# Optimization experiments

Hardware: AMD Instinct MI355X
Metric: run time of the kernel (lower is better)

## Reference

```python
import jax, jax.numpy as jnp
import numpy as np
import math

B, T, C = 2, 8192, 1024
H = 16
HD = C // H  # 64
WIN = 256    # local_window_size


def _rope_tables(T, hd):
    inv_freq = 1.0 / (10000.0 ** (np.arange(0, hd, 2, dtype=np.float32) / hd))
    t = np.arange(T, dtype=np.float32)
    freqs = np.outer(t, inv_freq)                      # [T, hd/2]
    emb = np.concatenate([freqs, freqs], axis=-1)      # [T, hd]
    return jnp.asarray(np.cos(emb))[None, None], jnp.asarray(np.sin(emb))[None, None]


def setup_inputs() -> dict:
    key = jax.random.key(0)
    ks = jax.random.split(key, 10)
    x = jax.random.normal(ks[0], (B, T, C), dtype=jnp.float32)
    # padding_mask: bool [B,T]; per the source, True positions end up masked out of attention
    padding_mask = jax.random.randint(ks[1], (B, T), 0, 2).astype(bool)
    cos, sin = _rope_tables(T, HD)                     # [1,1,T,HD]
    s = 1.0 / math.sqrt(C)
    Wq = jax.random.normal(ks[2], (C, C), dtype=jnp.float32) * s
    bq = jnp.zeros((C,), dtype=jnp.float32)
    Wk = jax.random.normal(ks[3], (C, C), dtype=jnp.float32) * s
    bk = jnp.zeros((C,), dtype=jnp.float32)
    Wv = jax.random.normal(ks[4], (C, C), dtype=jnp.float32) * s
    bv = jnp.zeros((C,), dtype=jnp.float32)
    Wo = jax.random.normal(ks[5], (C, C), dtype=jnp.float32) * s
    bo = jnp.zeros((C,), dtype=jnp.float32)
    return {"x": x, "padding_mask": padding_mask, "cos": cos, "sin": sin,
            "Wq": Wq, "bq": bq, "Wk": Wk, "bk": bk, "Wv": Wv, "bv": bv,
            "Wo": Wo, "bo": bo}


def _rotate_half(t):
    h = t.shape[-1] // 2
    return jnp.concatenate([-t[..., h:], t[..., :h]], axis=-1)


def reference(x, padding_mask, cos, sin, Wq, bq, Wk, bk, Wv, bv, Wo, bo):
    Bx, Tx, Cx = x.shape
    Wn = WIN
    pad_end = (Wn - Tx % Wn) % Wn            # static python int
    Tp = Tx + pad_end
    nW = Tp // Wn
    half = Wn // 2
    hd = cos.shape[-1]

    cos_t = jnp.broadcast_to(cos[0, 0][None], (Bx, Tx, hd))
    sin_t = jnp.broadcast_to(sin[0, 0][None], (Bx, Tx, hd))
    if pad_end > 0:
        x = jnp.pad(x, ((0, 0), (0, pad_end), (0, 0)))
        padding_mask = jnp.pad(padding_mask, ((0, 0), (0, pad_end)))
        cos_t = jnp.pad(cos_t, ((0, 0), (0, pad_end), (0, 0)))
        sin_t = jnp.pad(sin_t, ((0, 0), (0, pad_end), (0, 0)))

    # non-overlapping query windows: [B*nW, W, C]
    q_win = x.reshape(Bx * nW, Wn, Cx)
    cos_q = cos_t.reshape(Bx * nW, Wn, hd)[:, None]   # [Bw,1,W,hd]
    sin_q = sin_t.reshape(Bx * nW, Wn, hd)[:, None]

    # overlapping key/value windows of size 2W, stride W
    x_ctx = jnp.pad(x, ((0, 0), (half, half), (0, 0)))
    cos_ctx = jnp.pad(cos_t, ((0, 0), (half, half), (0, 0)))
    sin_ctx = jnp.pad(sin_t, ((0, 0), (half, half), (0, 0)))
    pk = jnp.pad(padding_mask, ((0, 0), (half, half)))  # pad value False
    idx = jnp.arange(nW)[:, None] * Wn + jnp.arange(2 * Wn)[None, :]  # [nW, 2W]
    k_win = x_ctx[:, idx].reshape(Bx * nW, 2 * Wn, Cx)
    cos_k = cos_ctx[:, idx].reshape(Bx * nW, 2 * Wn, hd)[:, None]
    sin_k = sin_ctx[:, idx].reshape(Bx * nW, 2 * Wn, hd)[:, None]
    pk = pk[:, idx].reshape(Bx * nW, 2 * Wn)

    # attn_mask: True = attend (SDPA bool-mask convention)
    attn_mask = ~pk
    all_attend = jnp.all(attn_mask, axis=-1)
    attn_mask = attn_mask.at[:, 0].set(jnp.where(all_attend, False, attn_mask[:, 0]))

    Bw = Bx * nW
    q = (q_win @ Wq.T + bq).reshape(Bw, Wn, H, HD).transpose(0, 2, 1, 3)        # [Bw,H,W,hd]
    k = (k_win @ Wk.T + bk).reshape(Bw, 2 * Wn, H, HD).transpose(0, 2, 1, 3)    # [Bw,H,2W,hd]
    v = (k_win @ Wv.T + bv).reshape(Bw, 2 * Wn, H, HD).transpose(0, 2, 1, 3)

    q = q * cos_q + _rotate_half(q) * sin_q
    k = k * cos_k + _rotate_half(k) * sin_k

    scale = 1.0 / math.sqrt(HD)
    scores = jnp.einsum('bhqd,bhkd->bhqk', q, k) * scale                        # [Bw,H,W,2W]
    scores = jnp.where(attn_mask[:, None, None, :], scores, jnp.finfo(scores.dtype).min)
    attn = jax.nn.softmax(scores, axis=-1)
    out = jnp.einsum('bhqk,bhkd->bhqd', attn, v)
    out = out.transpose(0, 2, 1, 3).reshape(Bw, Wn, Cx)
    out = out @ Wo.T + bo
    out = out.reshape(Bx, nW * Wn, Cx)[:, :Tx]
    return out
```

## Files before the change

### kernel.cpp

```cpp
#include <hip/hip_runtime.h>
#include <hip/hip_bf16.h>
#include <stdint.h>

#define T_SEQ 8192
#define B_SZ 2
#define CDIM 1024
#define NH 16
#define HDIM 64
#define NW 32

typedef unsigned short ushort_t;
typedef __attribute__((ext_vector_type(8))) short short8;
typedef __attribute__((ext_vector_type(8))) unsigned short us8;
typedef __attribute__((ext_vector_type(4))) unsigned short us4;
typedef __attribute__((ext_vector_type(4))) float f32x4;

__device__ __forceinline__ unsigned short f2bf(float f) {
  union { float f; unsigned int u; } c; c.f = f;
  return (unsigned short)((c.u + 0x7FFFu + ((c.u >> 16) & 1u)) >> 16);
}
__device__ __forceinline__ void gld16(void* lds, const void* g) {
  __builtin_amdgcn_global_load_lds(
      (const __attribute__((address_space(1))) void*)g,
      (__attribute__((address_space(3))) void*)lds, 16, 0, 0);
}

__global__ __launch_bounds__(256) void cvt_f32_bf16(const float* __restrict__ src,
                                                    ushort_t* __restrict__ dst, int n4)
{
  int i = blockIdx.x * 256 + threadIdx.x;
  if (i < n4) {
    float4 v = ((const float4*)src)[i];
    ushort4 o;
    o.x = f2bf(v.x); o.y = f2bf(v.y); o.z = f2bf(v.z); o.w = f2bf(v.w);
    ((ushort4*)dst)[i] = o;
  }
}

__global__ __launch_bounds__(256) void cvt_w4(const float* __restrict__ w0,
                                              const float* __restrict__ w1,
                                              const float* __restrict__ w2,
                                              const float* __restrict__ w3,
                                              ushort_t* __restrict__ dst)
{
  const float* srcs[4] = {w0, w1, w2, w3};
  const float* s = srcs[blockIdx.y];
  ushort_t* d = dst + (size_t)blockIdx.y * CDIM * CDIM;
  int i = blockIdx.x * 256 + threadIdx.x;
  float4 v = ((const float4*)s)[i];
  ushort4 o;
  o.x = f2bf(v.x); o.y = f2bf(v.y); o.z = f2bf(v.z); o.w = f2bf(v.w);
  ((ushort4*)d)[i] = o;
}

template <int EPI>
__global__ __launch_bounds__(256) void gemm_bt(const ushort_t* __restrict__ A,
                                               const ushort_t* __restrict__ W,
                                               const float* __restrict__ bias,
                                               void* __restrict__ OutP,
                                               const float* __restrict__ cosT,
                                               const float* __restrict__ sinT)
{
  __shared__ ushort_t As[128 * 32];
  __shared__ ushort_t Bs[128 * 32];
  const int t = threadIdx.x;
  const int lane = t & 63;
  const int wv = t >> 6;
  const int m0 = blockIdx.y * 128;
  const int n0 = blockIdx.x * 128;
  const int wm = (wv >> 1) * 64;
  const int wn = (wv & 1) * 64;

  f32x4 acc[4][4];
#pragma unroll
  for (int i = 0; i < 4; i++)
#pragma unroll
    for (int j = 0; j < 4; j++) acc[i][j] = (f32x4){0.f, 0.f, 0.f, 0.f};

  const int srow = t >> 2;
  const int scol = (t & 3) * 8;
  const ushort_t* Ag0 = A + (size_t)(m0 + srow) * CDIM + scol;
  const ushort_t* Ag1 = Ag0 + (size_t)64 * CDIM;
  const ushort_t* Wg0 = W + (size_t)(n0 + srow) * CDIM + scol;
  const ushort_t* Wg1 = Wg0 + (size_t)64 * CDIM;
  ushort_t* la0 = &As[srow * 32 + scol];
  ushort_t* la1 = &As[(srow + 64) * 32 + scol];
  ushort_t* lb0 = &Bs[srow * 32 + scol];
  ushort_t* lb1 = &Bs[(srow + 64) * 32 + scol];

  const int fr = lane & 15;
  const int kq = (lane >> 4) * 8;

  for (int kt = 0; kt < CDIM; kt += 32) {
    __syncthreads();
    gld16(la0, Ag0 + kt);
    gld16(la1, Ag1 + kt);
    gld16(lb0, Wg0 + kt);
    gld16(lb1, Wg1 + kt);
    __syncthreads();
    short8 a[4], b[4];
#pragma unroll
    for (int i = 0; i < 4; i++) a[i] = *(const short8*)&As[(wm + i * 16 + fr) * 32 + kq];
#pragma unroll
    for (int i = 0; i < 4; i++) b[i] = *(const short8*)&Bs[(wn + i * 16 + fr) * 32 + kq];
#pragma unroll
    for (int i = 0; i < 4; i++)
#pragma unroll
      for (int j = 0; j < 4; j++)
        acc[i][j] = __builtin_amdgcn_mfma_f32_16x16x32_bf16(a[i], b[j], acc[i][j], 0, 0, 0);
  }

  const int quad = lane >> 4;

  if constexpr (EPI == 1) {
    ushort_t* Out = (ushort_t*)OutP;
#pragma unroll
    for (int jp = 0; jp < 2; jp++) {
      int n_lo = n0 + wn + jp * 16 + fr;
      int n_hi = n_lo + 32;
      float bl = bias[n_lo], bh = bias[n_hi];
      int d = jp * 16 + fr;
#pragma unroll
      for (int i = 0; i < 4; i++) {
        int m = m0 + wm + i * 16 + quad * 4;
#pragma unroll
        for (int r = 0; r < 4; r++) {
          int tt = (m + r) & (T_SEQ - 1);
          float c = cosT[tt * HDIM + d];
          float sn = sinT[tt * HDIM + d];
          float lo = acc[i][jp][r] + bl;
          float hi = acc[i][jp + 2][r] + bh;
          Out[(size_t)(m + r) * CDIM + n_lo] = f2bf(lo * c - hi * sn);
          Out[(size_t)(m + r) * CDIM + n_hi] = f2bf(hi * c + lo * sn);
        }
      }
    }
  } else if constexpr (EPI == 2) {
    ushort_t* Out = (ushort_t*)OutP;
#pragma unroll
    for (int j = 0; j < 4; j++) {
      int n = n0 + wn + j * 16 + fr;
      float bvv = bias[n];
#pragma unroll
      for (int i = 0; i < 4; i++) {
        int m = m0 + wm + i * 16 + quad * 4;
        int bb = m >> 13;
        int tq = m & (T_SEQ - 1);
        us4 pk;
#pragma unroll
        for (int r = 0; r < 4; r++) pk[r] = f2bf(acc[i][j][r] + bvv);
        *(us4*)&Out[((size_t)bb * CDIM + n) * T_SEQ + tq] = pk;
      }
    }
  } else {
#pragma unroll
    for (int j = 0; j < 4; j++) {
      int n = n0 + wn + j * 16 + fr;
      float bvv = bias[n];
#pragma unroll
      for (int i = 0; i < 4; i++) {
        int m = m0 + wm + i * 16 + quad * 4;
#pragma unroll
        for (int r = 0; r < 4; r++) {
          if constexpr (EPI == 3)
            ((float*)OutP)[(size_t)(m + r) * CDIM + n] = acc[i][j][r] + bvv;
          else
            ((ushort_t*)OutP)[(size_t)(m + r) * CDIM + n] = f2bf(acc[i][j][r] + bvv);
        }
      }
    }
  }
}

__global__ __launch_bounds__(256) void attn_kernel(const ushort_t* __restrict__ Q,
                                                   const ushort_t* __restrict__ Kg,
                                                   const ushort_t* __restrict__ Vt,
                                                   const int* __restrict__ mask,
                                                   ushort_t* __restrict__ AO)
{
  __shared__ ushort_t Qs[128 * 72];
  __shared__ ushort_t Ks[64 * 72];
  __shared__ ushort_t Vts[64 * 72];
  __shared__ ushort_t Ps[4 * 16 * 72];
  __shared__ unsigned char att[512];

  const int t = threadIdx.x;
  const int lane = t & 63;
  const int wv = t >> 6;
  const int h = blockIdx.x;
  const int w = blockIdx.y >> 1;
  const int qh = blockIdx.y & 1;
  const int b = blockIdx.z;

  bool a0, a1;
  {
    int p0 = w * 256 + t - 128;
    a0 = (p0 < 0 || p0 >= T_SEQ) ? true : (mask[b * T_SEQ + p0] == 0);
    int p1 = p0 + 256;
    a1 = (p1 < 0 || p1 >= T_SEQ) ? true : (mask[b * T_SEQ + p1] == 0);
  }
  int all1 = __syncthreads_and((int)(a0 && a1));
  att[t] = a0 ? 1 : 0;
  att[t + 256] = a1 ? 1 : 0;
  if (all1 && t == 0) att[0] = 0;

  {
    int row = t >> 3;
    int c8 = (t & 7) * 8;
    size_t qbase = ((size_t)b * T_SEQ + w * 256 + qh * 128) * CDIM + h * HDIM + c8;
#pragma unroll
    for (int p = 0; p < 4; p++) {
      int r = p * 32 + row;
      *(us8*)&Qs[r * 72 + c8] = *(const us8*)&Q[qbase + (size_t)r * CDIM];
    }
  }

  const int fr = lane & 15;
  const int quad = lane >> 4;
  const int kq = quad * 8;
  const ushort_t* vt_base = Vt + ((size_t)b * CDIM + h * HDIM) * T_SEQ;

  float m_run[2][4], l_run[2][4];
  f32x4 o[2][4];
#pragma unroll
  for (int mt = 0; mt < 2; mt++)
#pragma unroll
    for (int r = 0; r < 4; r++) { m_run[mt][r] = -3.0e38f; l_run[mt][r] = 0.f; }
#pragma unroll
  for (int mt = 0; mt < 2; mt++)
#pragma unroll
    for (int nt = 0; nt < 4; nt++) o[mt][nt] = (f32x4){0.f, 0.f, 0.f, 0.f};

  for (int kc = 0; kc < 8; kc++) {
    __syncthreads();
    {
      int row = t >> 3;
      int c8 = (t & 7) * 8;
#pragma unroll
      for (int p = 0; p < 2; p++) {
        int jj = p * 32 + row;
        int pos = w * 256 + kc * 64 + jj - 128;
        us8 kval = (us8)(0);
        if (pos >= 0 && pos < T_SEQ)
          kval = *(const us8*)&Kg[((size_t)b * T_SEQ + pos) * CDIM + h * HDIM + c8];
        *(us8*)&Ks[jj * 72 + c8] = kval;
      }
    }
    {
      int dd = t >> 3;
      int kg = (t & 7) * 8;
      int pos0 = w * 256 + kc * 64 - 128 + kg;
      bool inr = (pos0 >= 0) && (pos0 < T_SEQ);
#pragma unroll
      for (int p = 0; p < 2; p++) {
        int d = p * 32 + dd;
        us8 vv = (us8)(0);
        if (inr) vv = *(const us8*)&vt_base[(size_t)d * T_SEQ + pos0];
        *(us8*)&Vts[d * 72 + kg] = vv;
      }
    }
    __syncthreads();

    short8 afr[2][2], bfr[4][2];
#pragma unroll
    for (int mt = 0; mt < 2; mt++)
#pragma unroll
      for (int ks = 0; ks < 2; ks++)
        afr[mt][ks] = *(const short8*)&Qs[(wv * 32 + mt * 16 + fr) * 72 + ks * 32 + kq];
#pragma unroll
    for (int nt = 0; nt < 4; nt++)
#pragma unroll
      for (int ks = 0; ks < 2; ks++)
        bfr[nt][ks] = *(const short8*)&Ks[(nt * 16 + fr) * 72 + ks * 32 + kq];

    f32x4 s[2][4];
#pragma unroll
    for (int mt = 0; mt < 2; mt++)
#pragma unroll
      for (int nt = 0; nt < 4; nt++) {
        f32x4 a = (f32x4){0.f, 0.f, 0.f, 0.f};
        a = __builtin_amdgcn_mfma_f32_16x16x32_bf16(afr[mt][0], bfr[nt][0], a, 0, 0, 0);
        a = __builtin_amdgcn_mfma_f32_16x16x32_bf16(afr[mt][1], bfr[nt][1], a, 0, 0, 0);
        s[mt][nt] = a;
      }

    bool at[4];
#pragma unroll
    for (int nt = 0; nt < 4; nt++) at[nt] = att[kc * 64 + nt * 16 + fr] != 0;
#pragma unroll
    for (int mt = 0; mt < 2; mt++)
#pragma unroll
      for (int nt = 0; nt < 4; nt++)
#pragma unroll
        for (int r = 0; r < 4; r++)
          s[mt][nt][r] = at[nt] ? s[mt][nt][r] * 0.125f : -3.0e38f;

#pragma unroll
    for (int mt = 0; mt < 2; mt++) {
#pragma unroll
      for (int r = 0; r < 4; r++) {
        float mm = fmaxf(fmaxf(s[mt][0][r], s[mt][1][r]), fmaxf(s[mt][2][r], s[mt][3][r]));
        for (int off = 1; off < 16; off <<= 1) mm = fmaxf(mm, __shfl_xor(mm, off, 64));
        float mnew = fmaxf(m_run[mt][r], mm);
        float alpha = __expf(m_run[mt][r] - mnew);
        float rs = 0.f;
#pragma unroll
        for (int nt = 0; nt < 4; nt++) {
          float p = __expf(s[mt][nt][r] - mnew);
          s[mt][nt][r] = p;
          rs += p;
        }
        for (int off = 1; off < 16; off <<= 1) rs += __shfl_xor(rs, off, 64);
        l_run[mt][r] = l_run[mt][r] * alpha + rs;
        m_run[mt][r] = mnew;
#pragma unroll
        for (int nt = 0; nt < 4; nt++) o[mt][nt][r] *= alpha;
      }
    }

    short8 vf[4][2];
#pragma unroll
    for (int nt = 0; nt < 4; nt++)
#pragma unroll
      for (int ks = 0; ks < 2; ks++)
        vf[nt][ks] = *(const short8*)&Vts[(nt * 16 + fr) * 72 + ks * 32 + kq];

    ushort_t* pw = &Ps[wv * 16 * 72];
    const int rot_r = 8 * (fr >> 2);
#pragma unroll
    for (int mt = 0; mt < 2; mt++) {
#pragma unroll
      for (int nt = 0; nt < 4; nt++) {
#pragma unroll
        for (int r = 0; r < 4; r++) {
          int cs = ((nt * 16 + fr) + 8 * quad) & 63;
          pw[(quad * 4 + r) * 72 + cs] = f2bf(s[mt][nt][r]);
        }
      }
      short8 pf[2];
#pragma unroll
      for (int ks = 0; ks < 2; ks++)
        pf[ks] = *(const short8*)&pw[fr * 72 + ((ks * 32 + kq + rot_r) & 63)];
#pragma unroll
      for (int nt = 0; nt < 4; nt++) {
        o[mt][nt] = __builtin_amdgcn_mfma_f32_16x16x32_bf16(pf[0], vf[nt][0], o[mt][nt], 0, 0, 0);
        o[mt][nt] = __builtin_amdgcn_mfma_f32_16x16x32_bf16(pf[1], vf[nt][1], o[mt][nt], 0, 0, 0);
      }
    }
  }

  size_t obase = ((size_t)b * T_SEQ + w * 256 + qh * 128) * CDIM + h * HDIM;
#pragma unroll
  for (int mt = 0; mt < 2; mt++)
#pragma unroll
    for (int r = 0; r < 4; r++) {
      int row = wv * 32 + mt * 16 + quad * 4 + r;
      float inv = 1.0f / fmaxf(l_run[mt][r], 1e-30f);
#pragma unroll
      for (int nt = 0; nt < 4; nt++) {
        int col = nt * 16 + fr;
        AO[obase + (size_t)row * CDIM + col] = f2bf(o[mt][nt][r] * inv);
      }
    }
}

extern "C" void kernel_launch(void* const* d_in, const int* in_sizes, int n_in,
                              void* d_out, int out_size, void* d_ws, size_t ws_size,
                              hipStream_t stream)
{
  const float* x    = (const float*)d_in[0];
  const int*   pm   = (const int*)d_in[1];
  const float* cosT = (const float*)d_in[2];
  const float* sinT = (const float*)d_in[3];
  const float* Wq   = (const float*)d_in[4];
  const float* bq   = (const float*)d_in[5];
  const float* Wk   = (const float*)d_in[6];
  const float* bk   = (const float*)d_in[7];
  const float* Wv   = (const float*)d_in[8];
  const float* bv   = (const float*)d_in[9];
  const float* Wo   = (const float*)d_in[10];
  const float* bo   = (const float*)d_in[11];
  float* out = (float*)d_out;

  const size_t NTOK = (size_t)B_SZ * T_SEQ;
  const size_t NELT = NTOK * CDIM;
  ushort_t* Kb  = (ushort_t*)d_out;
  ushort_t* xbf = (ushort_t*)d_out + NELT;
  char* ws = (char*)d_ws;
  ushort_t* Wbf = (ushort_t*)ws;
  ushort_t* Qb  = (ushort_t*)(ws + 4 * (size_t)CDIM * CDIM * 2);
  ushort_t* Vtb = Qb + NELT;
  ushort_t* AO  = Qb;

  cvt_f32_bf16<<<(int)(NELT / 4 / 256), 256, 0, stream>>>(x, xbf, (int)(NELT / 4));
  cvt_w4<<<dim3(CDIM * CDIM / 4 / 256, 4), 256, 0, stream>>>(Wq, Wk, Wv, Wo, Wbf);

  dim3 gg(CDIM / 128, (int)(NTOK / 128));
  const size_t WSZ = (size_t)CDIM * CDIM;
  gemm_bt<1><<<gg, 256, 0, stream>>>(xbf, Wbf + 0 * WSZ, bq, Qb,  cosT, sinT);
  gemm_bt<1><<<gg, 256, 0, stream>>>(xbf, Wbf + 1 * WSZ, bk, Kb,  cosT, sinT);
  gemm_bt<2><<<gg, 256, 0, stream>>>(xbf, Wbf + 2 * WSZ, bv, Vtb, nullptr, nullptr);

  attn_kernel<<<dim3(NH, NW * 2, B_SZ), 256, 0, stream>>>(Qb, Kb, Vtb, pm, AO);

  gemm_bt<3><<<gg, 256, 0, stream>>>(AO, Wbf + 3 * WSZ, bo, out, nullptr, nullptr);
}
```

Before: 485.9 us.

## Fuse QKV GEMMs, swizzle LDS with K=64 tiles, exp2 softmax

Merges the three Q/K/V projection launches into one kernel over a concatenated weight matrix and picks bias and epilogue by column section. The shared GEMM core now uses 64-wide K tiles with an XOR-swizzled LDS layout to cut bank conflicts and halve the barrier count. The Q/K RoPE epilogue stages results through LDS so global stores are coalesced 16-byte writes. Attention folds scale and mask into one FMA with a log2e-prescaled constant and uses exp2. The extra LDS use raises per-block footprint, and launch bounds now request 4 blocks per CU.

```diff
diff --git a/kernel.cpp b/kernel.cpp
--- a/kernel.cpp
+++ b/kernel.cpp
@@ -53,23 +53,77 @@
   ((ushort4*)d)[i] = o;
 }
 
-template <int EPI>
-__global__ __launch_bounds__(256) void gemm_bt(const ushort_t* __restrict__ A,
-                                               const ushort_t* __restrict__ W,
-                                               const float* __restrict__ bias,
-                                               void* __restrict__ OutP,
-                                               const float* __restrict__ cosT,
-                                               const float* __restrict__ sinT)
-{
-  __shared__ ushort_t As[128 * 32];
-  __shared__ ushort_t Bs[128 * 32];
+__device__ __forceinline__ void gemm_core(const ushort_t* __restrict__ A,
+                                          const ushort_t* __restrict__ W,
+                                          ushort_t* As, ushort_t* Bs,
+                                          int m0, int n0, int t, f32x4 acc[4][4])
+{
+  const int lane = t & 63;
+  const int wv = t >> 6;
+  const int wm = (wv >> 1) * 64;
+  const int wn = (wv & 1) * 64;
+  const int fr = lane & 15;
+  const int quad = lane >> 4;
+
+  const int srow = t >> 3;
+  const int sc8 = ((t & 7) ^ (srow & 7)) * 8;
+  const ushort_t* Ag = A + (size_t)(m0 + srow) * CDIM + sc8;
+  const ushort_t* Wg = W + (size_t)(n0 + srow) * CDIM + sc8;
+  ushort_t* lA = &As[srow * 64 + (t & 7) * 8];
+  ushort_t* lB = &Bs[srow * 64 + (t & 7) * 8];
+
+  for (int kt = 0; kt < CDIM; kt += 64) {
+    __syncthreads();
+#pragma unroll
+    for (int p = 0; p < 4; p++) gld16(lA + p * 2048, Ag + (size_t)p * 32 * CDIM + kt);
+#pragma unroll
+    for (int p = 0; p < 4; p++) gld16(lB + p * 2048, Wg + (size_t)p * 32 * CDIM + kt);
+    __syncthreads();
+#pragma unroll
+    for (int ks = 0; ks < 2; ks++) {
+      short8 a[4], b[4];
+#pragma unroll
+      for (int i = 0; i < 4; i++)
+        a[i] = *(const short8*)&As[(wm + i * 16 + fr) * 64 + (((ks * 4 + quad) ^ (fr & 7)) * 8)];
+#pragma unroll
+      for (int j = 0; j < 4; j++)
+        b[j] = *(const short8*)&Bs[(wn + j * 16 + fr) * 64 + (((ks * 4 + quad) ^ (fr & 7)) * 8)];
+#pragma unroll
+      for (int i = 0; i < 4; i++)
+#pragma unroll
+        for (int j = 0; j < 4; j++)
+          acc[i][j] = __builtin_amdgcn_mfma_f32_16x16x32_bf16(a[i], b[j], acc[i][j], 0, 0, 0);
+    }
+  }
+}
+
+__global__ __launch_bounds__(256, 4) void gemm_qkv(const ushort_t* __restrict__ A,
+                                                   const ushort_t* __restrict__ Wcat,
+                                                   const float* __restrict__ bq,
+                                                   const float* __restrict__ bk,
+                                                   const float* __restrict__ bv,
+                                                   ushort_t* __restrict__ Qb,
+                                                   ushort_t* __restrict__ Kb,
+                                                   ushort_t* __restrict__ Vtb,
+                                                   const float* __restrict__ cosT,
+                                                   const float* __restrict__ sinT)
+{
+  __shared__ ushort_t SH[17408];
+  ushort_t* As = SH;
+  ushort_t* Bs = SH + 8192;
+
   const int t = threadIdx.x;
   const int lane = t & 63;
   const int wv = t >> 6;
+  const int wm = (wv >> 1) * 64;
+  const int wn = (wv & 1) * 64;
+  const int fr = lane & 15;
+  const int quad = lane >> 4;
   const int m0 = blockIdx.y * 128;
   const int n0 = blockIdx.x * 128;
-  const int wm = (wv >> 1) * 64;
-  const int wn = (wv & 1) * 64;
+  const int sec = blockIdx.x >> 3;
+  const int nsec0 = (blockIdx.x & 7) * 128;
+  const float* bias = (sec == 0) ? bq : (sec == 1) ? bk : bv;
 
   f32x4 acc[4][4];
 #pragma unroll
@@ -77,70 +131,47 @@
 #pragma unroll
     for (int j = 0; j < 4; j++) acc[i][j] = (f32x4){0.f, 0.f, 0.f, 0.f};
 
-  const int srow = t >> 2;
-  const int scol = (t & 3) * 8;
-  const ushort_t* Ag0 = A + (size_t)(m0 + srow) * CDIM + scol;
-  const ushort_t* Ag1 = Ag0 + (size_t)64 * CDIM;
-  const ushort_t* Wg0 = W + (size_t)(n0 + srow) * CDIM + scol;
-  const ushort_t* Wg1 = Wg0 + (size_t)64 * CDIM;
-  ushort_t* la0 = &As[srow * 32 + scol];
-  ushort_t* la1 = &As[(srow + 64) * 32 + scol];
-  ushort_t* lb0 = &Bs[srow * 32 + scol];
-  ushort_t* lb1 = &Bs[(srow + 64) * 32 + scol];
-
-  const int fr = lane & 15;
-  const int kq = (lane >> 4) * 8;
-
-  for (int kt = 0; kt < CDIM; kt += 32) {
-    __syncthreads();
-    gld16(la0, Ag0 + kt);
-    gld16(la1, Ag1 + kt);
-    gld16(lb0, Wg0 + kt);
-    gld16(lb1, Wg1 + kt);
-    __syncthreads();
-    short8 a[4], b[4];
-#pragma unroll
-    for (int i = 0; i < 4; i++) a[i] = *(const short8*)&As[(wm + i * 16 + fr) * 32 + kq];
-#pragma unroll
-    for (int i = 0; i < 4; i++) b[i] = *(const short8*)&Bs[(wn + i * 16 + fr) * 32 + kq];
-#pragma unroll
-    for (int i = 0; i < 4; i++)
-#pragma unroll
-      for (int j = 0; j < 4; j++)
-        acc[i][j] = __builtin_amdgcn_mfma_f32_16x16x32_bf16(a[i], b[j], acc[i][j], 0, 0, 0);
-  }
-
-  const int quad = lane >> 4;
-
-  if constexpr (EPI == 1) {
-    ushort_t* Out = (ushort_t*)OutP;
+  gemm_core(A, Wcat, As, Bs, m0, n0, t, acc);
+
+  __syncthreads();
+
+  if (sec < 2) {
+    ushort_t* OutQK = sec ? Kb : Qb;
 #pragma unroll
     for (int jp = 0; jp < 2; jp++) {
-      int n_lo = n0 + wn + jp * 16 + fr;
-      int n_hi = n_lo + 32;
-      float bl = bias[n_lo], bh = bias[n_hi];
       int d = jp * 16 + fr;
+      int cl = wn + jp * 16 + fr;
+      float bl = bias[nsec0 + cl];
+      float bh = bias[nsec0 + cl + 32];
 #pragma unroll
       for (int i = 0; i < 4; i++) {
-        int m = m0 + wm + i * 16 + quad * 4;
+        int rloc = wm + i * 16 + quad * 4;
 #pragma unroll
         for (int r = 0; r < 4; r++) {
-          int tt = (m + r) & (T_SEQ - 1);
+          int tt = (m0 + rloc + r) & (T_SEQ - 1);
           float c = cosT[tt * HDIM + d];
           float sn = sinT[tt * HDIM + d];
           float lo = acc[i][jp][r] + bl;
           float hi = acc[i][jp + 2][r] + bh;
-          Out[(size_t)(m + r) * CDIM + n_lo] = f2bf(lo * c - hi * sn);
-          Out[(size_t)(m + r) * CDIM + n_hi] = f2bf(hi * c + lo * sn);
+          SH[(rloc + r) * 136 + cl] = f2bf(lo * c - hi * sn);
+          SH[(rloc + r) * 136 + cl + 32] = f2bf(hi * c + lo * sn);
         }
       }
     }
-  } else if constexpr (EPI == 2) {
-    ushort_t* Out = (ushort_t*)OutP;
+    __syncthreads();
+    const int rr0 = t >> 4;
+    const int c8 = (t & 15) * 8;
+    size_t gbase = (size_t)m0 * CDIM + nsec0 + c8;
+#pragma unroll
+    for (int p = 0; p < 8; p++) {
+      int rr = p * 16 + rr0;
+      *(us8*)&OutQK[gbase + (size_t)rr * CDIM] = *(const us8*)&SH[rr * 136 + c8];
+    }
+  } else {
 #pragma unroll
     for (int j = 0; j < 4; j++) {
-      int n = n0 + wn + j * 16 + fr;
-      float bvv = bias[n];
+      int ch = nsec0 + wn + j * 16 + fr;
+      float bvv = bias[ch];
 #pragma unroll
       for (int i = 0; i < 4; i++) {
         int m = m0 + wm + i * 16 + quad * 4;
@@ -149,25 +180,49 @@
         us4 pk;
 #pragma unroll
         for (int r = 0; r < 4; r++) pk[r] = f2bf(acc[i][j][r] + bvv);
-        *(us4*)&Out[((size_t)bb * CDIM + n) * T_SEQ + tq] = pk;
-      }
-    }
-  } else {
-#pragma unroll
-    for (int j = 0; j < 4; j++) {
-      int n = n0 + wn + j * 16 + fr;
-      float bvv = bias[n];
-#pragma unroll
-      for (int i = 0; i < 4; i++) {
-        int m = m0 + wm + i * 16 + quad * 4;
-#pragma unroll
-        for (int r = 0; r < 4; r++) {
-          if constexpr (EPI == 3)
-            ((float*)OutP)[(size_t)(m + r) * CDIM + n] = acc[i][j][r] + bvv;
-          else
-            ((ushort_t*)OutP)[(size_t)(m + r) * CDIM + n] = f2bf(acc[i][j][r] + bvv);
-        }
-      }
+        *(us4*)&Vtb[((size_t)bb * CDIM + ch) * T_SEQ + tq] = pk;
+      }
+    }
+  }
+}
+
+__global__ __launch_bounds__(256, 4) void gemm_out(const ushort_t* __restrict__ A,
+                                                   const ushort_t* __restrict__ W,
+                                                   const float* __restrict__ bias,
+                                                   float* __restrict__ Out)
+{
+  __shared__ ushort_t SH[16384];
+  ushort_t* As = SH;
+  ushort_t* Bs = SH + 8192;
+
+  const int t = threadIdx.x;
+  const int lane = t & 63;
+  const int wv = t >> 6;
+  const int wm = (wv >> 1) * 64;
+  const int wn = (wv & 1) * 64;
+  const int fr = lane & 15;
+  const int quad = lane >> 4;
+  const int m0 = blockIdx.y * 128;
+  const int n0 = blockIdx.x * 128;
+
+  f32x4 acc[4][4];
+#pragma unroll
+  for (int i = 0; i < 4; i++)
+#pragma unroll
+    for (int j = 0; j < 4; j++) acc[i][j] = (f32x4){0.f, 0.f, 0.f, 0.f};
+
+  gemm_core(A, W, As, Bs, m0, n0, t, acc);
+
+#pragma unroll
+  for (int j = 0; j < 4; j++) {
+    int n = n0 + wn + j * 16 + fr;
+    float bvv = bias[n];
+#pragma unroll
+    for (int i = 0; i < 4; i++) {
+      int m = m0 + wm + i * 16 + quad * 4;
+#pragma unroll
+      for (int r = 0; r < 4; r++)
+        Out[(size_t)(m + r) * CDIM + n] = acc[i][j][r] + bvv;
     }
   }
 }
@@ -219,6 +274,7 @@
   const int quad = lane >> 4;
   const int kq = quad * 8;
   const ushort_t* vt_base = Vt + ((size_t)b * CDIM + h * HDIM) * T_SEQ;
+  const float SCL = 0.18033688011112042f;
 
   float m_run[2][4], l_run[2][4];
   f32x4 o[2][4];
@@ -284,16 +340,17 @@
         s[mt][nt] = a;
       }
 
-    bool at[4];
-#pragma unroll
-    for (int nt = 0; nt < 4; nt++) at[nt] = att[kc * 64 + nt * 16 + fr] != 0;
+    float kb[4];
+#pragma unroll
+    for (int nt = 0; nt < 4; nt++)
+      kb[nt] = att[kc * 64 + nt * 16 + fr] ? 0.f : -1.0e38f;
 #pragma unroll
     for (int mt = 0; mt < 2; mt++)
 #pragma unroll
       for (int nt = 0; nt < 4; nt++)
 #pragma unroll
         for (int r = 0; r < 4; r++)
-          s[mt][nt][r] = at[nt] ? s[mt][nt][r] * 0.125f : -3.0e38f;
+          s[mt][nt][r] = __builtin_fmaf(s[mt][nt][r], SCL, kb[nt]);
 
 #pragma unroll
     for (int mt = 0; mt < 2; mt++) {
@@ -302,11 +359,11 @@
         float mm = fmaxf(fmaxf(s[mt][0][r], s[mt][1][r]), fmaxf(s[mt][2][r], s[mt][3][r]));
         for (int off = 1; off < 16; off <<= 1) mm = fmaxf(mm, __shfl_xor(mm, off, 64));
         float mnew = fmaxf(m_run[mt][r], mm);
-        float alpha = __expf(m_run[mt][r] - mnew);
+        float alpha = __builtin_amdgcn_exp2f(m_run[mt][r] - mnew);
         float rs = 0.f;
 #pragma unroll
         for (int nt = 0; nt < 4; nt++) {
-          float p = __expf(s[mt][nt][r] - mnew);
+          float p = __builtin_amdgcn_exp2f(s[mt][nt][r] - mnew);
           s[mt][nt][r] = p;
           rs += p;
         }
@@ -395,13 +452,11 @@
   cvt_f32_bf16<<<(int)(NELT / 4 / 256), 256, 0, stream>>>(x, xbf, (int)(NELT / 4));
   cvt_w4<<<dim3(CDIM * CDIM / 4 / 256, 4), 256, 0, stream>>>(Wq, Wk, Wv, Wo, Wbf);
 
-  dim3 gg(CDIM / 128, (int)(NTOK / 128));
-  const size_t WSZ = (size_t)CDIM * CDIM;
-  gemm_bt<1><<<gg, 256, 0, stream>>>(xbf, Wbf + 0 * WSZ, bq, Qb,  cosT, sinT);
-  gemm_bt<1><<<gg, 256, 0, stream>>>(xbf, Wbf + 1 * WSZ, bk, Kb,  cosT, sinT);
-  gemm_bt<2><<<gg, 256, 0, stream>>>(xbf, Wbf + 2 * WSZ, bv, Vtb, nullptr, nullptr);
+  gemm_qkv<<<dim3(24, (int)(NTOK / 128)), 256, 0, stream>>>(
+      xbf, Wbf, bq, bk, bv, Qb, Kb, Vtb, cosT, sinT);
 
   attn_kernel<<<dim3(NH, NW * 2, B_SZ), 256, 0, stream>>>(Qb, Kb, Vtb, pm, AO);
 
-  gemm_bt<3><<<gg, 256, 0, stream>>>(AO, Wbf + 3 * WSZ, bo, out, nullptr, nullptr);
-}
+  gemm_out<<<dim3(8, (int)(NTOK / 128)), 256, 0, stream>>>(
+      AO, Wbf + 3 * (size_t)CDIM * CDIM, bo, out);
+}
```

After: 451.4 us. 7.1% less time.
